# Optimization experiments

Hardware: AMD Instinct MI355X
Metric: run time of the kernel (lower is better)

## Reference

```python
import jax, jax.numpy as jnp
import numpy as np

N_NODES = 100000
N_EDGES = 1600000
IN_DIM = 128
EMB = 64
HID = 2 * EMB  # 128


def gcn_conv(x, W, b, row, col, norm):
    # PyG GCNConv: h = x @ W, then aggregate norm-weighted messages src->dst, then +bias
    h = x @ W                                   # [N, out]
    msg = norm[:, None] * h[row]                # gather over source nodes [E', out]
    out = jax.ops.segment_sum(msg, col, num_segments=N_NODES)  # scatter to targets
    return out + b


def gcn_norm(edge_index, edge_weight, n_nodes):
    # add self-loops with weight 1, then symmetric normalization D^-1/2 A D^-1/2
    loop = jnp.arange(n_nodes, dtype=edge_index.dtype)
    row = jnp.concatenate([edge_index[0], loop])
    col = jnp.concatenate([edge_index[1], loop])
    ew = jnp.concatenate([edge_weight, jnp.ones((n_nodes,), edge_weight.dtype)])
    deg = jax.ops.segment_sum(ew, col, num_segments=n_nodes)
    dinv = jnp.where(deg > 0, jax.lax.rsqrt(deg), 0.0)
    norm = dinv[row] * ew * dinv[col]
    return row, col, norm


def setup_inputs() -> dict:
    key = jax.random.key(0)
    ks = jax.random.split(key, 10)
    x = jax.random.normal(ks[0], (N_NODES, IN_DIM), dtype=jnp.float32)
    edge_index = jax.random.randint(ks[1], (2, N_EDGES), 0, N_NODES, dtype=jnp.int64)
    edge_weight = jax.random.uniform(ks[2], (N_EDGES,), dtype=jnp.float32)
    s1 = 1.0 / np.sqrt(IN_DIM)
    s2 = 1.0 / np.sqrt(HID)
    W1 = jax.random.uniform(ks[3], (IN_DIM, HID), jnp.float32, -s1, s1)
    b1 = jnp.zeros((HID,), jnp.float32)
    Wmu = jax.random.uniform(ks[4], (HID, EMB), jnp.float32, -s2, s2)
    bmu = jnp.zeros((EMB,), jnp.float32)
    Wlv = jax.random.uniform(ks[5], (HID, EMB), jnp.float32, -s2, s2)
    blv = jnp.zeros((EMB,), jnp.float32)
    return {"x": x, "edge_index": edge_index, "edge_weight": edge_weight,
            "W1": W1, "b1": b1, "Wmu": Wmu, "bmu": bmu, "Wlv": Wlv, "blv": blv}


def reference(x, edge_index, edge_weight, W1, b1, Wmu, bmu, Wlv, blv):
    row, col, norm = gcn_norm(edge_index, edge_weight, N_NODES)
    h = jax.nn.relu(gcn_conv(x, W1, b1, row, col, norm))
    mu = gcn_conv(h, Wmu, bmu, row, col, norm)
    logvar = gcn_conv(h, Wlv, blv, row, col, norm)
    return (mu, logvar)
```

## Files before the change

kernel.cpp:

```cpp
#include <hip/hip_runtime.h>

#define NN 100000
#define NE 1600000
#define DD 128
#define OUT_HALF 6400000
#define CAP 64

#define NB 256
#define NPB 391
#define BCAP 8192
#define BSTRIDE 64
#define CHUNK 2048
#define CPT 8

#define GNM 64
#define XPITCH 140

typedef unsigned int uint_t;
typedef float v4f __attribute__((ext_vector_type(4)));
typedef short v8s __attribute__((ext_vector_type(8)));

__device__ __forceinline__ unsigned short f2bf(float f) {
    uint_t u = __float_as_uint(f);
    u = (u + 0x7fffu + ((u >> 16) & 1u)) >> 16;
    return (unsigned short)u;
}
__device__ __forceinline__ float bf2f(unsigned short h) {
    return __uint_as_float(((uint_t)h) << 16);
}
__device__ __forceinline__ float bf_lo(uint_t u) { return __uint_as_float(u << 16); }
__device__ __forceinline__ float bf_hi(uint_t u) { return __uint_as_float(u & 0xffff0000u); }

#define EW_SCALE 32767.0f
#define EW_INV (1.0f / 32767.0f)


__global__ void k_zero(int* __restrict__ bcnt) {
    int i = blockIdx.x * blockDim.x + threadIdx.x;
    if (i < NB * BSTRIDE) bcnt[i] = 0;
}

__launch_bounds__(256)
__global__ void k_bin(const int* __restrict__ row, const int* __restrict__ col,
                      const float* __restrict__ ew, int* __restrict__ bcnt,
                      uint2* __restrict__ bins) {
    __shared__ uint2 sorted[CHUNK];
    __shared__ int hist[NB];
    __shared__ int lstart[NB];
    __shared__ int offs[NB];
    __shared__ int gbase[NB];
    const int tid = threadIdx.x;
    const int ebase = blockIdx.x * CHUNK;
    const int nloc = (NE - ebase < CHUNK) ? (NE - ebase) : CHUNK;

    hist[tid] = 0;
    __syncthreads();

    uint_t cols[CPT];
#pragma unroll
    for (int k = 0; k < CPT; ++k) {
        int i = ebase + k * 256 + tid;
        cols[k] = (i < NE) ? (uint_t)col[i] : 0xffffffffu;
        if (i < NE) atomicAdd(&hist[cols[k] / NPB], 1);
    }
    __syncthreads();

    int v = hist[tid];
#pragma unroll
    for (int s = 1; s < NB; s <<= 1) {
        int t = (tid >= s) ? hist[tid - s] : 0;
        __syncthreads();
        hist[tid] += t;
        __syncthreads();
    }
    int excl = hist[tid] - v;
    lstart[tid] = excl;
    offs[tid] = excl;
    gbase[tid] = atomicAdd(&bcnt[tid * BSTRIDE], v);
    __syncthreads();

#pragma unroll
    for (int k = 0; k < CPT; ++k) {
        int i = ebase + k * 256 + tid;
        if (i < NE) {
            uint_t c = cols[k];
            uint_t r = (uint_t)row[i];
            uint_t q = (uint_t)__float2int_rn(ew[i] * EW_SCALE);
            int pos = atomicAdd(&offs[c / NPB], 1);
            sorted[pos] = make_uint2((r << 15) | q, c);
        }
    }
    __syncthreads();

    for (int i = tid; i < nloc; i += 256) {
        uint2 rec = sorted[i];
        uint_t b = rec.y / NPB;
        int dst = gbase[b] + (i - lstart[b]);
        if (dst < BCAP) bins[(size_t)b * BCAP + dst] = rec;
    }
}


__launch_bounds__(512)
__global__ void k_scatter(const int* __restrict__ bcnt, const uint2* __restrict__ bins,
                          int* __restrict__ cnt, uint_t* __restrict__ slots,
                          float* __restrict__ dinv) {
    __shared__ int combo[NPB];
    const int b = blockIdx.x;
    const int tid = threadIdx.x;
    if (tid < NPB) combo[tid] = 0;
    __syncthreads();
    int n = bcnt[b * BSTRIDE];
    n = (n < BCAP) ? n : BCAP;
    const int base = b * NPB;
    const uint2* seg = bins + (size_t)b * BCAP;
    for (int i = tid; i < n; i += 512) {
        uint2 rec = seg[i];
        int lc = (int)rec.y - base;
        uint_t w = rec.x & 0x7fffu;
        uint_t old = (uint_t)atomicAdd(&combo[lc], (int)((1u << 22) | w));
        uint_t pos = old >> 22;
        if (pos < CAP) slots[rec.y * CAP + pos] = rec.x;
    }
    __syncthreads();
    if (tid < NPB) {
        int node = base + tid;
        if (node < NN) {
            uint_t v = (uint_t)combo[tid];
            int c = (int)(v >> 22);
            c = (c < CAP) ? c : CAP;
            int cp = (c + 15) & ~15;
            cnt[node] = cp;
            dinv[node] = rsqrtf(1.0f + (float)(v & 0x3fffffu) * EW_INV);
            uint_t padrec = (uint_t)node << 15;
            for (int j = c; j < cp; ++j) slots[node * CAP + j] = padrec;
        }
    }
}


template <bool RELU, bool OUT_BF16>
__launch_bounds__(256)
__global__ void k_gather(const uint_t* __restrict__ src, const int* __restrict__ cnt,
                         const uint_t* __restrict__ slots, const float* __restrict__ dinv,
                         const float* __restrict__ bias, void* __restrict__ dst) {
    int wid = (blockIdx.x * blockDim.x + threadIdx.x) >> 6;
    int lane = threadIdx.x & 63;
    if (wid >= NN) return;
    float di = dinv[wid];
    uint_t u = src[wid * 64 + lane];
    float accx = bf_lo(u);
    float accy = bf_hi(u);
    int end = __builtin_amdgcn_readfirstlane(cnt[wid]);
    const uint_t* seg = slots + wid * CAP;
    for (int jj = 0; jj < end; jj += 16) {
        uint_t rp[16];
#pragma unroll
        for (int q = 0; q < 16; ++q) rp[q] = seg[jj + q];
        uint_t sv[16];
#pragma unroll
        for (int q = 0; q < 16; ++q) sv[q] = src[(rp[q] >> 15) * 64 + lane];
#pragma unroll
        for (int q = 0; q < 16; ++q) {
            float p = (float)(rp[q] & 0x7fffu) * EW_INV;
            accx = fmaf(p, bf_lo(sv[q]), accx);
            accy = fmaf(p, bf_hi(sv[q]), accy);
        }
    }
    accx *= di;
    accy *= di;
    if (RELU) {
        float2 b = ((const float2*)bias)[lane];
        accx = fmaxf(accx + b.x, 0.0f) * di;
        accy = fmaxf(accy + b.y, 0.0f) * di;
    }
    if (OUT_BF16) {
        ((uint_t*)dst)[wid * 64 + lane] =
            (uint_t)f2bf(accx) | ((uint_t)f2bf(accy) << 16);
    } else {
        ((float2*)dst)[wid * 64 + lane] = make_float2(accx, accy);
    }
}


__global__ void k_wpack1(const float* __restrict__ W, unsigned short* __restrict__ P) {
    int e = blockIdx.x * blockDim.x + threadIdx.x;
    if (e >= 2048) return;
    int ln = e & 15, nt = (e >> 4) & 7, la = (e >> 7) & 3, kt = e >> 9;
    v8s v;
#pragma unroll
    for (int j = 0; j < 8; ++j) {
        int k = kt * 32 + la * 4 + (j & 3) + 16 * (j >> 2);
        v[j] = (short)f2bf(W[k * 128 + nt * 16 + ln]);
    }
    *(v8s*)&P[e * 8] = v;
}

__global__ void k_wpack2(const float* __restrict__ Wmu, const float* __restrict__ Wlv,
                         unsigned short* __restrict__ P) {
    int e = blockIdx.x * blockDim.x + threadIdx.x;
    if (e >= 2048) return;
    int ln = e & 15, nt = (e >> 4) & 7, la = (e >> 7) & 3, kt = e >> 9;
    v8s v;
#pragma unroll
    for (int j = 0; j < 8; ++j) {
        int k = kt * 32 + la * 4 + (j & 3) + 16 * (j >> 2);
        float f = (nt < 4) ? Wmu[k * 64 + nt * 16 + ln]
                           : Wlv[k * 64 + (nt - 4) * 16 + ln];
        v[j] = (short)f2bf(f);
    }
    *(v8s*)&P[e * 8] = v;
}


__launch_bounds__(256)
__global__ void k_gemm_h0(const float* __restrict__ X,
                          const unsigned short* __restrict__ Wpk,
                          const float* __restrict__ dinv,
                          unsigned short* __restrict__ Y) {
    __shared__ float xs[GNM * XPITCH];
    const int tid = threadIdx.x;
    const int node0 = blockIdx.x * GNM;

    {
        const float4* X4 = (const float4*)X;
        for (int i = tid; i < GNM * 32; i += 256) {
            int row = i >> 5, kg = i & 31;
            int ne = node0 + row;
            if (ne >= NN) ne = NN - 1;
            *(float4*)&xs[row * XPITCH + kg * 4] = X4[ne * 32 + kg];
        }
    }
    __syncthreads();

    const int wave = tid >> 6, lane = tid & 63;
    const int la = lane >> 4, ln = lane & 15;
    const float* xrow = &xs[(wave * 16 + ln) * XPITCH];
    const v8s* Wf = (const v8s*)Wpk;

    v4f acc[8];
#pragma unroll
    for (int nt = 0; nt < 8; ++nt) acc[nt] = (v4f){0.f, 0.f, 0.f, 0.f};

    for (int kt = 0; kt < 4; ++kt) {
        float4 xa0 = *(const float4*)&xrow[kt * 32 + la * 4];
        float4 xa1 = *(const float4*)&xrow[kt * 32 + la * 4 + 16];
        float xv[8] = {xa0.x, xa0.y, xa0.z, xa0.w, xa1.x, xa1.y, xa1.z, xa1.w};
        v8s ah, al;
#pragma unroll
        for (int j = 0; j < 8; ++j) {
            unsigned short h = f2bf(xv[j]);
            ah[j] = (short)h;
            al[j] = (short)f2bf(xv[j] - bf2f(h));
        }
        const int wbase = (kt * 4 + la) * 8 * 16;
#pragma unroll
        for (int nt = 0; nt < 8; ++nt) {
            v8s bh = Wf[wbase + nt * 16 + ln];
            acc[nt] = __builtin_amdgcn_mfma_f32_16x16x32_bf16(ah, bh, acc[nt], 0, 0, 0);
            acc[nt] = __builtin_amdgcn_mfma_f32_16x16x32_bf16(al, bh, acc[nt], 0, 0, 0);
        }
    }

#pragma unroll
    for (int r = 0; r < 4; ++r) {
        int node = node0 + wave * 16 + la * 4 + r;
        if (node < NN) {
            float di = dinv[node];
#pragma unroll
            for (int nt = 0; nt < 8; ++nt)
                Y[node * 128 + nt * 16 + ln] = f2bf(acc[nt][r] * di);
        }
    }
}

__launch_bounds__(256)
__global__ void k_gemm_out(const float* __restrict__ G,
                           const unsigned short* __restrict__ Wpk,
                           const float* __restrict__ bmu, const float* __restrict__ blv,
                           float* __restrict__ out) {
    __shared__ float xs[GNM * XPITCH];
    const int tid = threadIdx.x;
    const int node0 = blockIdx.x * GNM;

    {
        const float4* G4 = (const float4*)G;
        for (int i = tid; i < GNM * 32; i += 256) {
            int row = i >> 5, kg = i & 31;
            int ne = node0 + row;
            if (ne >= NN) ne = NN - 1;
            *(float4*)&xs[row * XPITCH + kg * 4] = G4[ne * 32 + kg];
        }
    }
    __syncthreads();

    const int wave = tid >> 6, lane = tid & 63;
    const int la = lane >> 4, ln = lane & 15;
    const float* xrow = &xs[(wave * 16 + ln) * XPITCH];
    const v8s* Wf = (const v8s*)Wpk;

    v4f acc[8];
#pragma unroll
    for (int nt = 0; nt < 8; ++nt) acc[nt] = (v4f){0.f, 0.f, 0.f, 0.f};

    for (int kt = 0; kt < 4; ++kt) {
        float4 xa0 = *(const float4*)&xrow[kt * 32 + la * 4];
        float4 xa1 = *(const float4*)&xrow[kt * 32 + la * 4 + 16];
        float xv[8] = {xa0.x, xa0.y, xa0.z, xa0.w, xa1.x, xa1.y, xa1.z, xa1.w};
        v8s ah, al;
#pragma unroll
        for (int j = 0; j < 8; ++j) {
            unsigned short h = f2bf(xv[j]);
            ah[j] = (short)h;
            al[j] = (short)f2bf(xv[j] - bf2f(h));
        }
        const int wbase = (kt * 4 + la) * 8 * 16;
#pragma unroll
        for (int nt = 0; nt < 8; ++nt) {
            v8s bh = Wf[wbase + nt * 16 + ln];
            acc[nt] = __builtin_amdgcn_mfma_f32_16x16x32_bf16(ah, bh, acc[nt], 0, 0, 0);
            acc[nt] = __builtin_amdgcn_mfma_f32_16x16x32_bf16(al, bh, acc[nt], 0, 0, 0);
        }
    }

    float bb[8];
#pragma unroll
    for (int nt = 0; nt < 8; ++nt)
        bb[nt] = (nt < 4) ? bmu[nt * 16 + ln] : blv[(nt - 4) * 16 + ln];

#pragma unroll
    for (int r = 0; r < 4; ++r) {
        int node = node0 + wave * 16 + la * 4 + r;
        if (node < NN) {
#pragma unroll
            for (int nt = 0; nt < 8; ++nt) {
                float v = acc[nt][r] + bb[nt];
                if (nt < 4)
                    out[node * 64 + nt * 16 + ln] = v;
                else
                    out[OUT_HALF + node * 64 + (nt - 4) * 16 + ln] = v;
            }
        }
    }
}


extern "C" void kernel_launch(void* const* d_in, const int* in_sizes, int n_in,
                              void* d_out, int out_size, void* d_ws, size_t ws_size,
                              hipStream_t stream) {
    const float* x   = (const float*)d_in[0];
    const int*   ei  = (const int*)d_in[1];
    const float* ew  = (const float*)d_in[2];
    const float* W1  = (const float*)d_in[3];
    const float* b1  = (const float*)d_in[4];
    const float* Wmu = (const float*)d_in[5];
    const float* bmu = (const float*)d_in[6];
    const float* Wlv = (const float*)d_in[7];
    const float* blv = (const float*)d_in[8];
    const int* rowi = ei;
    const int* coli = ei + NE;
    float* out = (float*)d_out;

    int*    cnt   = (int*)d_ws;
    float*  dinv  = (float*)(cnt + 100352);
    uint_t* slots = (uint_t*)(dinv + 100352);
    float*  poolA = (float*)(slots + NN * CAP);
    uint_t* y0    = (uint_t*)poolA;
    float*  g     = poolA;
    uint_t* y1    = (uint_t*)(poolA + NN * DD);
    uint2*  bins  = (uint2*)poolA;
    int*    bcnt  = (int*)(poolA + NB * BCAP * 2);
    unsigned short* Wpk1 = (unsigned short*)(poolA + NN * 64);
    unsigned short* Wpk2 = (unsigned short*)(poolA + NN * DD);

    const int B = 256;
    const int GGRID = (NN + GNM - 1) / GNM;
    k_zero<<<(NB * BSTRIDE + B - 1) / B, B, 0, stream>>>(bcnt);
    k_bin<<<(NE + CHUNK - 1) / CHUNK, B, 0, stream>>>(rowi, coli, ew, bcnt, bins);
    k_scatter<<<NB, 512, 0, stream>>>(bcnt, bins, cnt, slots, dinv);
    k_wpack1<<<8, B, 0, stream>>>(W1, Wpk1);
    k_gemm_h0<<<GGRID, B, 0, stream>>>(x, Wpk1, dinv, (unsigned short*)y0);
    k_gather<true, true><<<(NN * 64 + B - 1) / B, B, 0, stream>>>(
        y0, cnt, slots, dinv, b1, y1);
    k_gather<false, false><<<(NN * 64 + B - 1) / B, B, 0, stream>>>(
        y1, cnt, slots, dinv, b1, g);
    k_wpack2<<<8, B, 0, stream>>>(Wmu, Wlv, Wpk2);
    k_gemm_out<<<GGRID, B, 0, stream>>>(g, Wpk2, bmu, blv, out);
}
```

Before: 321.6 us.

## Fuse second-layer gather aggregation into output GEMM kernel

Removes the separate second gather pass that wrote an fp32 aggregated feature buffer to global memory. The output GEMM kernel now gathers neighbor bf16 rows itself, builds the aggregated tile in shared memory, then runs the MFMA GEMM. This saves one kernel launch and a full N×128 fp32 write and read. In exchange, each block serializes 16 nodes per wave through gathering, so fewer waves are in flight to hide latency. Wpk2 moves to the start of poolA, since that buffer is no longer used for g.

After: 317.5 us. About the same (-1.3%).

```diff
diff --git a/kernel.cpp b/kernel.cpp
--- a/kernel.cpp
+++ b/kernel.cpp
@@ -274,27 +274,50 @@
     }
 }
 
+
 __launch_bounds__(256)
-__global__ void k_gemm_out(const float* __restrict__ G,
-                           const unsigned short* __restrict__ Wpk,
-                           const float* __restrict__ bmu, const float* __restrict__ blv,
-                           float* __restrict__ out) {
+__global__ void k_gg_out(const uint_t* __restrict__ src, const int* __restrict__ cnt,
+                         const uint_t* __restrict__ slots, const float* __restrict__ dinv,
+                         const unsigned short* __restrict__ Wpk,
+                         const float* __restrict__ bmu, const float* __restrict__ blv,
+                         float* __restrict__ out) {
     __shared__ float xs[GNM * XPITCH];
     const int tid = threadIdx.x;
     const int node0 = blockIdx.x * GNM;
-
-    {
-        const float4* G4 = (const float4*)G;
-        for (int i = tid; i < GNM * 32; i += 256) {
-            int row = i >> 5, kg = i & 31;
-            int ne = node0 + row;
-            if (ne >= NN) ne = NN - 1;
-            *(float4*)&xs[row * XPITCH + kg * 4] = G4[ne * 32 + kg];
-        }
-    }
-    __syncthreads();
-
     const int wave = tid >> 6, lane = tid & 63;
+
+    for (int n = 0; n < 16; ++n) {
+        int node = node0 + wave * 16 + n;
+        float accx = 0.0f, accy = 0.0f;
+        if (node < NN) {
+            float di = dinv[node];
+            uint_t u = src[node * 64 + lane];
+            accx = bf_lo(u);
+            accy = bf_hi(u);
+            int end = __builtin_amdgcn_readfirstlane(cnt[node]);
+            const uint_t* seg = slots + node * CAP;
+            for (int jj = 0; jj < end; jj += 16) {
+                uint_t rp[16];
+#pragma unroll
+                for (int q = 0; q < 16; ++q) rp[q] = seg[jj + q];
+                uint_t sv[16];
+#pragma unroll
+                for (int q = 0; q < 16; ++q) sv[q] = src[(rp[q] >> 15) * 64 + lane];
+#pragma unroll
+                for (int q = 0; q < 16; ++q) {
+                    float p = (float)(rp[q] & 0x7fffu) * EW_INV;
+                    accx = fmaf(p, bf_lo(sv[q]), accx);
+                    accy = fmaf(p, bf_hi(sv[q]), accy);
+                }
+            }
+            accx *= di;
+            accy *= di;
+        }
+        xs[(wave * 16 + n) * XPITCH + lane * 2] = accx;
+        xs[(wave * 16 + n) * XPITCH + lane * 2 + 1] = accy;
+    }
+    __syncthreads();
+
     const int la = lane >> 4, ln = lane & 15;
     const float* xrow = &xs[(wave * 16 + ln) * XPITCH];
     const v8s* Wf = (const v8s*)Wpk;
@@ -366,12 +389,11 @@
     uint_t* slots = (uint_t*)(dinv + 100352);
     float*  poolA = (float*)(slots + NN * CAP);
     uint_t* y0    = (uint_t*)poolA;
-    float*  g     = poolA;
     uint_t* y1    = (uint_t*)(poolA + NN * DD);
     uint2*  bins  = (uint2*)poolA;
     int*    bcnt  = (int*)(poolA + NB * BCAP * 2);
     unsigned short* Wpk1 = (unsigned short*)(poolA + NN * 64);
-    unsigned short* Wpk2 = (unsigned short*)(poolA + NN * DD);
+    unsigned short* Wpk2 = (unsigned short*)poolA;
 
     const int B = 256;
     const int GGRID = (NN + GNM - 1) / GNM;
@@ -382,8 +404,6 @@
     k_gemm_h0<<<GGRID, B, 0, stream>>>(x, Wpk1, dinv, (unsigned short*)y0);
     k_gather<true, true><<<(NN * 64 + B - 1) / B, B, 0, stream>>>(
         y0, cnt, slots, dinv, b1, y1);
-    k_gather<false, false><<<(NN * 64 + B - 1) / B, B, 0, stream>>>(
-        y1, cnt, slots, dinv, b1, g);
     k_wpack2<<<8, B, 0, stream>>>(Wmu, Wlv, Wpk2);
-    k_gemm_out<<<GGRID, B, 0, stream>>>(g, Wpk2, bmu, blv, out);
-}
+    k_gg_out<<<GGRID, B, 0, stream>>>(y1, cnt, slots, dinv, Wpk2, bmu, blv, out);
+}
```
